# Performance work log

Measured on AMD Instinct MI355X. Metric: run time of the kernel, lower is better.

Reference implementation:

```python
import jax, jax.numpy as jnp
import numpy as np

STATE_DIM = 256
HID_DIM = 1024
BATCH = 65536
IN_DIM = 2 * STATE_DIM + 1


def setup_inputs() -> dict:
    key = jax.random.key(0)
    ks = jax.random.split(key, 11)
    x0 = jax.random.normal(ks[0], (BATCH, STATE_DIM), dtype=jnp.float32)
    x1 = jax.random.normal(ks[1], (BATCH, STATE_DIM), dtype=jnp.float32)
    t = jax.random.uniform(ks[2], (BATCH, 1), dtype=jnp.float32)

    def linear_init(k, fan_in, fan_out):
        kw, kb = jax.random.split(k)
        bound = 1.0 / np.sqrt(fan_in)
        W = jax.random.uniform(kw, (fan_in, fan_out), minval=-bound, maxval=bound, dtype=jnp.float32)
        b = jax.random.uniform(kb, (fan_out,), minval=-bound, maxval=bound, dtype=jnp.float32)
        return W, b

    W1, b1 = linear_init(ks[3], IN_DIM, HID_DIM)
    W2, b2 = linear_init(ks[4], HID_DIM, HID_DIM)
    W3, b3 = linear_init(ks[5], HID_DIM, HID_DIM)
    W4, b4 = linear_init(ks[6], HID_DIM, STATE_DIM)
    return {"x0": x0, "x1": x1, "t": t,
            "W1": W1, "b1": b1, "W2": W2, "b2": b2,
            "W3": W3, "b3": b3, "W4": W4, "b4": b4}


def _mlp(z, W1, b1, W2, b2, W3, b3, W4, b4):
    h = jax.nn.relu(z @ W1 + b1)
    h = jax.nn.relu(h @ W2 + b2)
    h = jax.nn.relu(h @ W3 + b3)
    return h @ W4 + b4  # [B, state_dim]


def reference(x0, x1, t, W1, b1, W2, b2, W3, b3, W4, b4):
    z = jnp.concatenate((x0, x1, t), axis=1)  # [B, 2*D+1]
    # d(fnn)/dt == last column of the per-sample Jacobian; compute it with one
    # forward-mode JVP using the one-hot tangent on the t slot (fuses with fwd).
    tz = jnp.zeros_like(z).at[:, -1].set(1.0)
    fnn, dt_fnn = jax.jvp(lambda zz: _mlp(zz, W1, b1, W2, b2, W3, b3, W4, b4), (z,), (tz,))
    xt = (1.0 - t) * x0 + t * x1 + t * (1.0 - t) * fnn
    dt_xt = x1 - x0 + (1.0 - t) * fnn - t * fnn + t * (1.0 - t) * dt_fnn
    return (xt, dt_xt)
```

## Files before the change

kernel.cpp:

```cpp
#include <hip/hip_runtime.h>
#include <stdint.h>
#include <stddef.h>


typedef unsigned short u16;
typedef __attribute__((ext_vector_type(8))) short short8;
typedef __attribute__((ext_vector_type(4))) float f32x4;

#define BATCH 65536
#define SDIM 256
#define HDIM 1024

__device__ __forceinline__ u16 f2bf(float f) {
  unsigned int u = __float_as_uint(f);
  u += 0x7FFFu + ((u >> 16) & 1u);
  return (u16)(u >> 16);
}

__device__ __forceinline__ void gload_lds16(const void* g, void* l) {
  __builtin_amdgcn_global_load_lds(
      (const __attribute__((address_space(1))) unsigned int*)g,
      (__attribute__((address_space(3))) unsigned int*)l, 16, 0, 0);
}

struct EpiArgs {
  const float* bias;
  const float* r1;
  const float* t;
  const float* x0;
  const float* x1;
  u16*   out_h;
  float* out_xt;
  float* out_dt;
};

template <int EPI>
__global__ __launch_bounds__(512, 2)
void fgemm8(const u16* __restrict__ A, const u16* __restrict__ Bt,
            int N, int K, EpiArgs e)
{
  __shared__ __align__(16) u16 lds[65536];

  const int tid  = threadIdx.x;
  const int wave = tid >> 6;
  const int lane = tid & 63;
  const int hi   = lane >> 4;
  const int ln   = lane & 15;
  const int srow = lane >> 3;
  const int ssc  = lane & 7;
  const int lcs  = (ssc ^ srow) * 8;

  const int nbx = gridDim.x;
  int bx = blockIdx.x, by = blockIdx.y;
  if ((gridDim.y & 7) == 0) {
    const int id = by * nbx + bx;
    const int g  = id & 7;
    const int s  = id >> 3;
    bx = s % nbx;
    by = (s / nbx) * 8 + g;
  }
  const int bn = bx * 256;
  const int bm = by * 256;

  const int wm = (wave >> 2) * 128;
  const int wn = (wave & 3) * 64;

  f32x4 acc[8][4] = {};

  const u16* gA = A  + (size_t)bm * K + lcs;
  const u16* gB = Bt + (size_t)bn * K + lcs;
  const int NT = K >> 6;

  auto STAGE = [&](int t) {
    const int kk0 = t << 6;
    const int lb  = (t & 1) << 15;
#pragma unroll
    for (int c = 0; c < 4; ++c) {
      const int ch  = (wave << 2) + c;
      const int row = (ch << 3) + srow;
      gload_lds16(gA + (size_t)row * K + kk0, &lds[lb + ch * 512]);
      gload_lds16(gB + (size_t)row * K + kk0, &lds[lb + 16384 + ch * 512]);
    }
  };

  STAGE(0);
  STAGE(1);

  for (int t = 0; t < NT; ++t) {
    if (t + 1 < NT) asm volatile("s_waitcnt vmcnt(8)" ::: "memory");
    else            asm volatile("s_waitcnt vmcnt(0)" ::: "memory");
    __builtin_amdgcn_s_barrier();
    __builtin_amdgcn_sched_barrier(0);

    const int lb = (t & 1) << 15;
#pragma unroll
    for (int kh = 0; kh < 2; ++kh) {
      const int scs = (((kh << 2) + hi) ^ (ln & 7)) * 8;
      short8 a8[8], b8[4];
#pragma unroll
      for (int i = 0; i < 8; ++i)
        a8[i] = *(const short8*)&lds[lb + (wm + i * 16 + ln) * 64 + scs];
#pragma unroll
      for (int j = 0; j < 4; ++j)
        b8[j] = *(const short8*)&lds[lb + 16384 + (wn + j * 16 + ln) * 64 + scs];
      __builtin_amdgcn_s_setprio(1);
#pragma unroll
      for (int i = 0; i < 8; ++i)
#pragma unroll
        for (int j = 0; j < 4; ++j)
          acc[i][j] = __builtin_amdgcn_mfma_f32_16x16x32_bf16(
              a8[i], b8[j], acc[i][j], 0, 0, 0);
      __builtin_amdgcn_s_setprio(0);
    }

    __builtin_amdgcn_sched_barrier(0);
    __builtin_amdgcn_s_barrier();
    __builtin_amdgcn_sched_barrier(0);
    if (t + 2 < NT) STAGE(t + 2);
  }

  if constexpr (EPI == 0) {
#pragma unroll
    for (int mi = 0; mi < 8; ++mi) {
#pragma unroll
      for (int ni = 0; ni < 4; ++ni) {
        const int n = bn + wn + ni * 16 + ln;
        const float bnv = e.bias[n];
        const float r1n = e.r1[n];
#pragma unroll
        for (int r = 0; r < 4; ++r) {
          const int m = bm + wm + mi * 16 + hi * 4 + r;
          const float pre = acc[mi][ni][r] + bnv + e.t[m] * r1n;
          const size_t sH = (size_t)(m >> 4) * 32 + (m & 15);
          e.out_h[sH * (size_t)N + n]        = f2bf(fmaxf(pre, 0.f));
          e.out_h[(sH + 16) * (size_t)N + n] = (pre > 0.f) ? f2bf(r1n) : (u16)0;
        }
      }
    }
  } else if constexpr (EPI == 1) {
#pragma unroll
    for (int j = 0; j < 4; ++j) {
#pragma unroll
      for (int ni = 0; ni < 4; ++ni) {
        const int n = bn + wn + ni * 16 + ln;
        const float bnv = e.bias[n];
#pragma unroll
        for (int r = 0; r < 4; ++r) {
          const size_t sH = (size_t)(bm + wm + j * 32 + hi * 4 + r);
          const float pre = acc[2 * j][ni][r] + bnv;
          const float vu  = acc[2 * j + 1][ni][r];
          e.out_h[sH * (size_t)N + n]        = f2bf(fmaxf(pre, 0.f));
          e.out_h[(sH + 16) * (size_t)N + n] = (pre > 0.f) ? f2bf(vu) : (u16)0;
        }
      }
    }
  } else {
#pragma unroll
    for (int j = 0; j < 4; ++j) {
#pragma unroll
      for (int ni = 0; ni < 4; ++ni) {
        const int n = bn + wn + ni * 16 + ln;
        const float bnv = e.bias[n];
#pragma unroll
        for (int r = 0; r < 4; ++r) {
          const int sH = bm + wm + j * 32 + hi * 4 + r;
          const int m  = ((sH >> 5) << 4) + (hi * 4 + r);
          const float fnn = acc[2 * j][ni][r] + bnv;
          const float dtf = acc[2 * j + 1][ni][r];
          const float tt  = e.t[m];
          const size_t ix = (size_t)m * 256 + n;
          const float a = e.x0[ix], b = e.x1[ix];
          const float w = tt * (1.f - tt);
          e.out_xt[ix] = (1.f - tt) * a + tt * b + w * fnn;
          e.out_dt[ix] = b - a + (1.f - 2.f * tt) * fnn + w * dtf;
        }
      }
    }
  }
}

__global__ void prep_z(const float* __restrict__ x0, const float* __restrict__ x1,
                       u16* __restrict__ A0)
{
  const int idx = blockIdx.x * blockDim.x + threadIdx.x;
  const int m = idx >> 7;
  const int c = idx & 127;
  const float* src = (c < 64) ? (x0 + (size_t)m * 256 + c * 4)
                              : (x1 + (size_t)m * 256 + (c - 64) * 4);
  const float4 v = *(const float4*)src;
  uint2 pk;
  pk.x = (unsigned)f2bf(v.x) | ((unsigned)f2bf(v.y) << 16);
  pk.y = (unsigned)f2bf(v.z) | ((unsigned)f2bf(v.w) << 16);
  *(uint2*)&A0[(size_t)m * 512 + c * 4] = pk;
}

__global__ void transpose_cast(const float* __restrict__ W, u16* __restrict__ Wt,
                               int K, int N)
{
  __shared__ float tile[32][33];
  const int tx = threadIdx.x & 31;
  const int ty = threadIdx.x >> 5;
  const int k0 = blockIdx.x * 32;
  const int n0 = blockIdx.y * 32;
#pragma unroll
  for (int i = 0; i < 32; i += 8)
    tile[ty + i][tx] = W[(size_t)(k0 + ty + i) * N + n0 + tx];
  __syncthreads();
#pragma unroll
  for (int i = 0; i < 32; i += 8)
    Wt[(size_t)(n0 + ty + i) * K + k0 + tx] = f2bf(tile[tx][ty + i]);
}

extern "C" void kernel_launch(void* const* d_in, const int* in_sizes, int n_in,
                              void* d_out, int out_size, void* d_ws, size_t ws_size,
                              hipStream_t stream)
{
  const float* x0 = (const float*)d_in[0];
  const float* x1 = (const float*)d_in[1];
  const float* t  = (const float*)d_in[2];
  const float* W1 = (const float*)d_in[3];
  const float* b1 = (const float*)d_in[4];
  const float* W2 = (const float*)d_in[5];
  const float* b2 = (const float*)d_in[6];
  const float* W3 = (const float*)d_in[7];
  const float* b3 = (const float*)d_in[8];
  const float* W4 = (const float*)d_in[9];
  const float* b4 = (const float*)d_in[10];

  char* ws = (char*)d_ws;
  const size_t WB1 = (size_t)512 * HDIM * 2;
  const size_t WB2 = (size_t)HDIM * HDIM * 2;
  const size_t WB4 = (size_t)HDIM * SDIM * 2;
  u16* Wt1 = (u16*)(ws);
  u16* Wt2 = (u16*)(ws + WB1);
  u16* Wt3 = (u16*)(ws + WB1 + WB2);
  u16* Wt4 = (u16*)(ws + WB1 + 2 * WB2);
  const size_t wmark = WB1 + 2 * WB2 + WB4;
  char* act = ws + wmark;

  int nc = 1;
  while (nc < 64 && wmark + (size_t)(BATCH / nc) * 8192 > ws_size) nc <<= 1;
  const int CB = BATCH / nc;

  u16* Sa = (u16*)(act);
  u16* Sb = (u16*)(act + (size_t)CB * 4096);
  u16* Zc = Sb;

  transpose_cast<<<dim3(16, 32), 256, 0, stream>>>(W1, Wt1, 512, HDIM);
  transpose_cast<<<dim3(32, 32), 256, 0, stream>>>(W2, Wt2, HDIM, HDIM);
  transpose_cast<<<dim3(32, 32), 256, 0, stream>>>(W3, Wt3, HDIM, HDIM);
  transpose_cast<<<dim3(32, 8),  256, 0, stream>>>(W4, Wt4, HDIM, SDIM);

  const float* r1 = W1 + (size_t)512 * HDIM;
  float* out_xt = (float*)d_out;
  float* out_dt = (float*)d_out + (size_t)BATCH * SDIM;

  for (int c = 0; c < nc; ++c) {
    const size_t mb = (size_t)c * CB;

    prep_z<<<(CB * 128) / 256, 256, 0, stream>>>(x0 + mb * SDIM, x1 + mb * SDIM, Zc);

    { EpiArgs e{}; e.bias = b1; e.r1 = r1; e.t = t + mb; e.out_h = Sa;
      fgemm8<0><<<dim3(HDIM / 256, CB / 256), 512, 0, stream>>>(Zc, Wt1, HDIM, 512, e); }

    { EpiArgs e{}; e.bias = b2; e.out_h = Sb;
      fgemm8<1><<<dim3(HDIM / 256, CB / 128), 512, 0, stream>>>(Sa, Wt2, HDIM, HDIM, e); }

    { EpiArgs e{}; e.bias = b3; e.out_h = Sa;
      fgemm8<1><<<dim3(HDIM / 256, CB / 128), 512, 0, stream>>>(Sb, Wt3, HDIM, HDIM, e); }

    { EpiArgs e{}; e.bias = b4; e.t = t + mb;
      e.x0 = x0 + mb * SDIM; e.x1 = x1 + mb * SDIM;
      e.out_xt = out_xt + mb * SDIM; e.out_dt = out_dt + mb * SDIM;
      fgemm8<2><<<dim3(SDIM / 256, CB / 128), 512, 0, stream>>>(Sa, Wt4, SDIM, HDIM, e); }
  }
}
```

Baseline: 1.096 ms.

## Restructure GEMM mainloop into 4-stage K=32 pipeline with split loads and barriers

Replaces the double-buffered K=64 tile loop with a four-buffer ring of K=32 tiles, prefetching three steps ahead and splitting each step's A and B loads across two half-iterations. Each iteration now runs two MFMA phases separated by barriers, interleaving LDS reads and global-to-LDS copies with compute at finer granularity, and uses a new XOR swizzle for the 32-wide rows. The goal is to hide global load latency and LDS read latency behind MFMA work. It adds more barriers per unit of work and relies on tricky hand-tuned vmcnt counts.

```diff
diff --git a/kernel.cpp b/kernel.cpp
--- a/kernel.cpp
+++ b/kernel.cpp
@@ -46,9 +46,9 @@
   const int lane = tid & 63;
   const int hi   = lane >> 4;
   const int ln   = lane & 15;
-  const int srow = lane >> 3;
-  const int ssc  = lane & 7;
-  const int lcs  = (ssc ^ srow) * 8;
+
+  const int srow4  = tid >> 2;
+  const int schunk = (tid & 3) ^ (srow4 & 3);
 
   const int nbx = gridDim.x;
   int bx = blockIdx.x, by = blockIdx.y;
@@ -67,56 +67,80 @@
 
   f32x4 acc[8][4] = {};
 
-  const u16* gA = A  + (size_t)bm * K + lcs;
-  const u16* gB = Bt + (size_t)bn * K + lcs;
-  const int NT = K >> 6;
-
-  auto STAGE = [&](int t) {
-    const int kk0 = t << 6;
-    const int lb  = (t & 1) << 15;
-#pragma unroll
-    for (int c = 0; c < 4; ++c) {
-      const int ch  = (wave << 2) + c;
-      const int row = (ch << 3) + srow;
-      gload_lds16(gA + (size_t)row * K + kk0, &lds[lb + ch * 512]);
-      gload_lds16(gB + (size_t)row * K + kk0, &lds[lb + 16384 + ch * 512]);
+  const int NH = K >> 5;
+
+  const u16* pA = A  + (size_t)(bm + srow4) * K + schunk * 8;
+  const u16* pB = Bt + (size_t)(bn + srow4) * K + schunk * 8;
+  const size_t rstep = (size_t)128 * K;
+
+  auto STAGE = [&](int q, int piece) {
+    const int base = ((q & 3) << 14) + (piece << 13) + tid * 8;
+    const u16* gp  = (piece ? pB : pA) + q * 32;
+#pragma unroll
+    for (int r = 0; r < 2; ++r)
+      gload_lds16(gp + r * rstep, &lds[base + r * 4096]);
+  };
+
+  const int slot = (hi ^ (ln & 3)) << 3;
+  int aoff[8], boff[4];
+#pragma unroll
+  for (int i = 0; i < 8; ++i) aoff[i] = (wm + i * 16 + ln) * 32 + slot;
+#pragma unroll
+  for (int j = 0; j < 4; ++j) boff[j] = 8192 + (wn + j * 16 + ln) * 32 + slot;
+
+  STAGE(0, 0); STAGE(0, 1);
+  STAGE(1, 0); STAGE(1, 1);
+  STAGE(2, 0); STAGE(2, 1);
+  asm volatile("s_waitcnt vmcnt(8)" ::: "memory");
+  __builtin_amdgcn_s_barrier();
+
+  for (int q = 0; q < NH; ++q) {
+    const int buf = (q & 3) << 14;
+
+    short8 a0[4], b0[4];
+#pragma unroll
+    for (int i = 0; i < 4; ++i) a0[i] = *(const short8*)&lds[buf + aoff[i]];
+#pragma unroll
+    for (int j = 0; j < 4; ++j) b0[j] = *(const short8*)&lds[buf + boff[j]];
+    if (q + 3 < NH) STAGE(q + 3, 0);
+    __builtin_amdgcn_sched_barrier(0);
+    __builtin_amdgcn_s_barrier();
+    asm volatile("s_waitcnt lgkmcnt(0)" ::: "memory");
+    __builtin_amdgcn_sched_barrier(0);
+    __builtin_amdgcn_s_setprio(1);
+#pragma unroll
+    for (int i = 0; i < 4; ++i)
+#pragma unroll
+      for (int j = 0; j < 4; ++j)
+        acc[i][j] = __builtin_amdgcn_mfma_f32_16x16x32_bf16(
+            a0[i], b0[j], acc[i][j], 0, 0, 0);
+    __builtin_amdgcn_s_setprio(0);
+    __builtin_amdgcn_sched_barrier(0);
+    __builtin_amdgcn_s_barrier();
+
+    short8 a1[4];
+#pragma unroll
+    for (int i = 0; i < 4; ++i) a1[i] = *(const short8*)&lds[buf + aoff[4 + i]];
+    if (q + 1 < NH) {
+      if (q < NH - 3)       asm volatile("s_waitcnt vmcnt(6)" ::: "memory");
+      else if (q == NH - 3) asm volatile("s_waitcnt vmcnt(4)" ::: "memory");
+      else                  asm volatile("s_waitcnt vmcnt(0)" ::: "memory");
     }
-  };
-
-  STAGE(0);
-  STAGE(1);
-
-  for (int t = 0; t < NT; ++t) {
-    if (t + 1 < NT) asm volatile("s_waitcnt vmcnt(8)" ::: "memory");
-    else            asm volatile("s_waitcnt vmcnt(0)" ::: "memory");
+    if (q + 3 < NH) STAGE(q + 3, 1);
+    __builtin_amdgcn_sched_barrier(0);
     __builtin_amdgcn_s_barrier();
-    __builtin_amdgcn_sched_barrier(0);
-
-    const int lb = (t & 1) << 15;
-#pragma unroll
-    for (int kh = 0; kh < 2; ++kh) {
-      const int scs = (((kh << 2) + hi) ^ (ln & 7)) * 8;
-      short8 a8[8], b8[4];
-#pragma unroll
-      for (int i = 0; i < 8; ++i)
-        a8[i] = *(const short8*)&lds[lb + (wm + i * 16 + ln) * 64 + scs];
+    asm volatile("s_waitcnt lgkmcnt(0)" ::: "memory");
+    __builtin_amdgcn_sched_barrier(0);
+    __builtin_amdgcn_s_setprio(1);
+#pragma unroll
+    for (int i = 0; i < 4; ++i)
 #pragma unroll
       for (int j = 0; j < 4; ++j)
-        b8[j] = *(const short8*)&lds[lb + 16384 + (wn + j * 16 + ln) * 64 + scs];
-      __builtin_amdgcn_s_setprio(1);
-#pragma unroll
-      for (int i = 0; i < 8; ++i)
-#pragma unroll
-        for (int j = 0; j < 4; ++j)
-          acc[i][j] = __builtin_amdgcn_mfma_f32_16x16x32_bf16(
-              a8[i], b8[j], acc[i][j], 0, 0, 0);
-      __builtin_amdgcn_s_setprio(0);
-    }
-
+        acc[4 + i][j] = __builtin_amdgcn_mfma_f32_16x16x32_bf16(
+            a1[i], b0[j], acc[4 + i][j], 0, 0, 0);
+    __builtin_amdgcn_s_setprio(0);
     __builtin_amdgcn_sched_barrier(0);
     __builtin_amdgcn_s_barrier();
-    __builtin_amdgcn_sched_barrier(0);
-    if (t + 2 < NT) STAGE(t + 2);
   }
 
   if constexpr (EPI == 0) {
```

Result: slower. 1.124 ms (+2.5%).
